# Performance work log

Hardware: AMD Instinct MI355X
Metric: run time of the kernel (lower is better)

## Reference

```python
import jax, jax.numpy as jnp
import numpy as np

N_NODES = 50000
N_EDGES = 500000
N_REL = 8
D = 128        # input_dim
A_DIM = 64     # attention_dim
D_OUT = 128    # output_dim


def setup_inputs() -> dict:
    key = jax.random.key(0)
    ks = jax.random.split(key, 10)
    h = jax.random.normal(ks[0], (N_NODES, D), jnp.float32)
    # relation gate tables: [R, 2*D, D]; first D rows act on dst (subject), last D on src (object)
    relations = jax.random.normal(ks[1], (N_REL, 2 * D, D), jnp.float32) * 0.05
    rel_attention = jax.random.normal(ks[2], (N_REL, A_DIM), jnp.float32) * 0.05
    W_a = jax.random.normal(ks[3], (A_DIM, 2 * D), jnp.float32) * 0.05
    b_a = jnp.zeros((A_DIM,), jnp.float32)
    W_lin = jax.random.normal(ks[4], (D_OUT, 2 * D), jnp.float32) * 0.05
    b_lin = jnp.zeros((D_OUT,), jnp.float32)
    src = jax.random.randint(ks[5], (N_EDGES,), 0, N_NODES, dtype=jnp.int32)
    dst = jax.random.randint(ks[6], (N_EDGES,), 0, N_NODES, dtype=jnp.int32)
    etype = jax.random.randint(ks[7], (N_EDGES,), 0, N_REL, dtype=jnp.int32)
    return {"h": h, "relations": relations, "rel_attention": rel_attention,
            "W_a": W_a, "b_a": b_a, "W_lin": W_lin, "b_lin": b_lin,
            "src": src, "dst": dst, "etype": etype}


def reference(h, relations, rel_attention, W_a, b_a, W_lin, b_lin, src, dst, etype):
    d = h.shape[-1]
    # --- gates: relation-indexed gather_mm (concat gate type) ---
    # Project every node through every relation once (R is small), then gather per edge.
    proj_dst = jnp.einsum('nd,rde->rne', h, relations[:, :d, :])   # [R, N, D] subject/dst side
    proj_src = jnp.einsum('nd,rde->rne', h, relations[:, d:, :])   # [R, N, D] object/src side
    gate = jax.nn.sigmoid(proj_dst[etype, dst] + proj_src[etype, src])  # [E, D]

    src_h = h[src]   # [E, D]
    dst_h = h[dst]   # [E, D]

    # --- gatv2 attention (predicates are zeroed in the module -> rel_attention[0]) ---
    a = jax.nn.leaky_relu(jnp.concatenate([dst_h, src_h], axis=-1) @ W_a.T + b_a)  # [E, A]
    score = (rel_attention[0] * a).sum(-1)  # [E]

    # --- edge_softmax over destination-node segments ---
    smax = jax.ops.segment_max(score, dst, num_segments=N_NODES)
    ex = jnp.exp(score - smax[dst])
    denom = jax.ops.segment_sum(ex, dst, num_segments=N_NODES)
    attn = ex / denom[dst]  # [E]

    # --- message = u_mul_e(h, attn*gate), reduce = sum over dst ---
    msg = src_h * (attn[:, None] * gate)                 # [E, D]
    h_N = jax.ops.segment_sum(msg, dst, num_segments=N_NODES)  # [N, D]

    # --- graphsage aggregate: LeakyReLU(W [h ; h_N] + b) ---
    out = jax.nn.leaky_relu(jnp.concatenate([h, h_N], axis=-1) @ W_lin.T + b_lin)
    return out
```

## Files before the change

### kernel.cpp

```cpp
#include <hip/hip_runtime.h>
#include <cstdint>
#include <cstddef>

constexpr int NNODES = 50000;
constexpr int NEDGES = 500000;
constexpr int NRELS  = 8;
constexpr int DIM    = 128;
constexpr int ADIM   = 64;
constexpr int TWOD   = 256;
constexpr int EPB    = 64;
constexpr float SLOPE = 0.01f;

constexpr int XPITCH = TWOD + 8;
constexpr int SPAD = NEDGES + 1024;

typedef __attribute__((ext_vector_type(8))) short short8;
typedef __attribute__((ext_vector_type(4))) float floatx4;

__device__ __forceinline__ unsigned short f2bf(float f) {
    unsigned u = __float_as_uint(f);
    unsigned r = u + 0x7FFFu + ((u >> 16) & 1u);
    return (unsigned short)(r >> 16);
}
__device__ __forceinline__ float bf2f(unsigned short b) {
    return __uint_as_float(((unsigned)b) << 16);
}
__device__ __forceinline__ float sigmoid_fast(float x) {
    return __builtin_amdgcn_rcpf(1.0f + __expf(-x));
}

typedef const __attribute__((address_space(1))) void* gas_ptr;
typedef __attribute__((address_space(3))) void* las_ptr;
__device__ __forceinline__ void gload_lds16(const void* g, void* l) {
    __builtin_amdgcn_global_load_lds((gas_ptr)g, (las_ptr)l, 16, 0, 0);
}

__global__ void k_init(int* __restrict__ histD, int* __restrict__ cursorD,
                       int* __restrict__ cnts) {
    int i = blockIdx.x * blockDim.x + threadIdx.x;
    int stride = gridDim.x * blockDim.x;
    for (int idx = i; idx < NNODES; idx += stride) { histD[idx] = 0; cursorD[idx] = 0; }
    if (i < 16) cnts[i] = 0;
}

__global__ __launch_bounds__(256) void k_prep(const float* __restrict__ rel,
                                              const float* __restrict__ W_lin,
                                              const float* __restrict__ W_a,
                                              unsigned short* __restrict__ relT,
                                              unsigned short* __restrict__ Wl,
                                              unsigned short* __restrict__ Wa16) {
    __shared__ float ls[64][65];
    int b = blockIdx.x, t = threadIdx.x;
    if (b < 64) {
        int r = b >> 3, tile = b & 7;
        int d0 = (tile >> 1) * 64, o0 = (tile & 1) * 64;
        const float* rp = rel + ((size_t)r * TWOD + d0) * DIM + o0;
#pragma unroll
        for (int u = 0; u < 16; u++) {
            int v = u * 256 + t;
            int j = v & 63, i = v >> 6;
            ls[i][j] = rp[(size_t)i * DIM + j];
        }
        __syncthreads();
        unsigned short* wp = relT + ((size_t)r * DIM + o0) * TWOD + d0;
#pragma unroll
        for (int u = 0; u < 16; u++) {
            int v = u * 256 + t;
            int ii = v & 63, jj = v >> 6;
            wp[(size_t)jj * TWOD + ii] = f2bf(ls[ii][jj]);
        }
    } else {
        int idx = (b - 64) * 256 + t;
        if (idx < DIM * TWOD) {
            Wl[idx] = f2bf(W_lin[idx]);
        } else {
            int j = idx - DIM * TWOD;
            if (j < ADIM * TWOD) Wa16[j] = f2bf(W_a[j]);
        }
    }
}

__global__ void k_h16(const float* __restrict__ h, unsigned short* __restrict__ h16) {
    int i = blockIdx.x * 256 + threadIdx.x;
    if (i < NNODES * DIM / 8) {
        const float4* hp = (const float4*)(h + (size_t)i * 8);
        float4 a = hp[0], b = hp[1];
        union { unsigned short us[8]; short8 s8; } pk;
        pk.us[0] = f2bf(a.x); pk.us[1] = f2bf(a.y); pk.us[2] = f2bf(a.z); pk.us[3] = f2bf(a.w);
        pk.us[4] = f2bf(b.x); pk.us[5] = f2bf(b.y); pk.us[6] = f2bf(b.z); pk.us[7] = f2bf(b.w);
        *(short8*)&h16[(size_t)i * 8] = pk.s8;
    }
}

__global__ void k_hist2(const int* __restrict__ ety, const int* __restrict__ dst,
                        int* __restrict__ cnt, int* __restrict__ histD) {
    __shared__ int hist[NRELS];
    int t = threadIdx.x;
    if (t < NRELS) hist[t] = 0;
    __syncthreads();
    int e = blockIdx.x * 256 + t;
    if (e < NEDGES) {
        atomicAdd(&hist[ety[e]], 1);
        atomicAdd(&histD[dst[e]], 1);
    }
    __syncthreads();
    if (t < NRELS && hist[t] > 0) atomicAdd(&cnt[t], hist[t]);
}

__global__ __launch_bounds__(1024) void k_scan(const int* __restrict__ histD,
                                               int* __restrict__ row_ptr,
                                               const int* __restrict__ cnt,
                                               int* __restrict__ offs,
                                               uint2* __restrict__ sMeta) {
    __shared__ int ls[1024];
    __shared__ int s_offs[NRELS + 1];
    __shared__ int s_cnt[NRELS];
    const int t = threadIdx.x;
    const int CH = (NNODES + 1023) / 1024;
    const int base = t * CH;
    int s = 0;
    for (int j = 0; j < CH; j++) { int i = base + j; if (i < NNODES) s += histD[i]; }
    ls[t] = s;
    __syncthreads();
    for (int off = 1; off < 1024; off <<= 1) {
        int v = (t >= off) ? ls[t - off] : 0;
        __syncthreads();
        ls[t] += v;
        __syncthreads();
    }
    int run = (t == 0) ? 0 : ls[t - 1];
    for (int j = 0; j < CH; j++) {
        int i = base + j;
        if (i < NNODES) { row_ptr[i] = run; run += histD[i]; }
    }
    if (t == 1023) row_ptr[NNODES] = ls[1023];
    if (t == 0) {
        int off = 0;
        for (int r = 0; r < NRELS; r++) {
            offs[r] = off; s_offs[r] = off; s_cnt[r] = cnt[r];
            off += ((cnt[r] + EPB - 1) / EPB) * EPB;
        }
        s_offs[NRELS] = off;
    }
    __syncthreads();
#pragma unroll
    for (int r = 0; r < NRELS; r++) {
        int s0 = s_offs[r] + s_cnt[r];
        int e0 = s_offs[r + 1 > NRELS ? NRELS : r + 1];
        for (int idx = s0 + t; idx < e0; idx += 1024) sMeta[idx] = make_uint2(0xFFFFFFFFu, 0u);
    }
    for (int idx = s_offs[NRELS] + t; idx < SPAD; idx += 1024)
        sMeta[idx] = make_uint2(0xFFFFFFFFu, 0u);
}

__global__ void k_escatter(const int* __restrict__ ety, const int* __restrict__ src,
                           const int* __restrict__ dst, const int* __restrict__ row_ptr,
                           const int* __restrict__ offs,
                           int* __restrict__ cursorD, int* __restrict__ cursorE,
                           uint2* __restrict__ sMeta) {
    __shared__ int hist[NRELS];
    __shared__ int basew[NRELS];
    int t = threadIdx.x;
    if (t < NRELS) hist[t] = 0;
    __syncthreads();
    int e = blockIdx.x * 256 + t;
    int r = -1, rank = 0, sn = 0, dn = 0;
    if (e < NEDGES) {
        r = ety[e]; sn = src[e]; dn = dst[e];
        rank = atomicAdd(&hist[r], 1);
    }
    __syncthreads();
    if (t < NRELS && hist[t] > 0) basew[t] = atomicAdd(&cursorE[t], hist[t]);
    __syncthreads();
    if (e < NEDGES) {
        int s = offs[r] + basew[r] + rank;
        int pos = row_ptr[dn] + atomicAdd(&cursorD[dn], 1);
        sMeta[s] = make_uint2((unsigned)sn | ((unsigned)dn << 16), (unsigned)pos);
    }
}

__global__ __launch_bounds__(256, 4) void k_gate_msg(
    const unsigned short* __restrict__ h16, const unsigned short* __restrict__ relT,
    const unsigned short* __restrict__ Wa16,
    const uint2* __restrict__ sMeta, const float* __restrict__ b_a,
    const float* __restrict__ ratt, const int* __restrict__ offs,
    unsigned short* __restrict__ msgbuf, float* __restrict__ scoreP) {
    __shared__ unsigned short Xs[EPB * 256];
    __shared__ int srcn_s[EPB];
    __shared__ int dstn_s[EPB];
    __shared__ int pos_s[EPB];
    __shared__ int val_s[EPB];
    __shared__ float scoreW[EPB][4];

    const int t = threadIdx.x;
    const int base = blockIdx.x * EPB;
    const int lane = t & 63;
    const int wave = t >> 6;

    if (t < EPB) {
        uint2 m2 = sMeta[base + t];
        int valid = (m2.x != 0xFFFFFFFFu);
        val_s[t] = valid;
        srcn_s[t] = valid ? (int)(m2.x & 0xFFFFu) : 0;
        dstn_s[t] = valid ? (int)(m2.x >> 16) : 0;
        pos_s[t] = valid ? (int)m2.y : 0;
    }
    __syncthreads();
    if (!val_s[0]) return;

    int r = 0;
#pragma unroll
    for (int i = 1; i < NRELS; i++) if (base >= offs[i]) r = i;

#pragma unroll
    for (int u = 0; u < 8; u++) {
        int j = wave * 8 + u;
        int row = j * 2 + (lane >> 5);
        int lu = (lane & 31) ^ (row & 7);
        int node = (lu < 16) ? dstn_s[row] : srcn_s[row];
        gload_lds16(&h16[(size_t)node * DIM + (lu & 15) * 8], &Xs[j * 512]);
    }

    const int q = lane >> 4;
    const int l16 = lane & 15;
    const int o16 = wave * 16 + l16;

    const unsigned short* bp0 = relT + ((size_t)r * DIM + (wave * 2 + 0) * 16 + l16) * TWOD + q * 8;
    const unsigned short* bp1 = relT + ((size_t)r * DIM + (wave * 2 + 1) * 16 + l16) * TWOD + q * 8;
    const unsigned short* wb  = Wa16 + (size_t)o16 * TWOD + q * 8;

    short8 B0p[8];
#pragma unroll
    for (int ks = 0; ks < 8; ks++) B0p[ks] = *(const short8*)(bp0 + ks * 32);
#pragma unroll
    for (int ks = 0; ks < 8; ks++) asm volatile("" :: "v"(B0p[ks]));

    __syncthreads();

    floatx4 acc[4][2];
    floatx4 accS[4];
#pragma unroll
    for (int m = 0; m < 4; m++) {
        acc[m][0] = (floatx4)(0.0f);
        acc[m][1] = (floatx4)(0.0f);
        accS[m] = (floatx4)(0.0f);
    }

#pragma unroll
    for (int ks = 0; ks < 8; ks++) {
        short8 B0 = B0p[ks];
        short8 B1 = *(const short8*)(bp1 + ks * 32);
        short8 BS = *(const short8*)(wb + ks * 32);
        short8 Af[4];
#pragma unroll
        for (int m = 0; m < 4; m++) {
            int row = m * 16 + l16;
            Af[m] = *(const short8*)&Xs[row * 256 + ((((ks * 4) + q) ^ (l16 & 7)) << 3)];
        }
#pragma unroll
        for (int m = 0; m < 4; m++) {
            acc[m][0] = __builtin_amdgcn_mfma_f32_16x16x32_bf16(Af[m], B0, acc[m][0], 0, 0, 0);
            acc[m][1] = __builtin_amdgcn_mfma_f32_16x16x32_bf16(Af[m], B1, acc[m][1], 0, 0, 0);
            accS[m]   = __builtin_amdgcn_mfma_f32_16x16x32_bf16(Af[m], BS, accS[m], 0, 0, 0);
        }
    }

    __syncthreads();

    {
        float ba = b_a[o16];
        float ra = ratt[o16];
#pragma unroll
        for (int m = 0; m < 4; m++) {
#pragma unroll
            for (int rg = 0; rg < 4; rg++) {
                float v = accS[m][rg] + ba;
                v = v > 0.0f ? v : SLOPE * v;
                v *= ra;
#pragma unroll
                for (int off = 8; off > 0; off >>= 1) v += __shfl_xor(v, off, 16);
                if (l16 == 0) scoreW[m * 16 + q * 4 + rg][wave] = v;
            }
        }
    }

#pragma unroll
    for (int m = 0; m < 4; m++) {
        int ib = m * 16 + q * 4;
#pragma unroll
        for (int nn = 0; nn < 2; nn++) {
            int o = (wave * 2 + nn) * 16 + l16;
            int uS = 16 + (o >> 3), uD = o >> 3, ofs = o & 7;
#pragma unroll
            for (int rg = 0; rg < 4; rg++) {
                int i = ib + rg;
                float g = sigmoid_fast(acc[m][nn][rg]);
                float sh = bf2f(Xs[i * 256 + ((uS ^ (i & 7)) << 3) + ofs]);
                Xs[i * 256 + ((uD ^ (i & 7)) << 3) + ofs] = f2bf(sh * g);
            }
        }
    }
    __syncthreads();

#pragma unroll
    for (int u = 0; u < 4; u++) {
        int v = u * 256 + t;
        int i = v >> 4;
        int c = v & 15;
        if (!val_s[i]) continue;
        short8 val = *(const short8*)&Xs[i * 256 + ((c ^ (i & 7)) << 3)];
        *(short8*)&msgbuf[(size_t)pos_s[i] * DIM + c * 8] = val;
    }
    if (t < EPB && val_s[t]) {
        scoreP[pos_s[t]] = scoreW[t][0] + scoreW[t][1] + scoreW[t][2] + scoreW[t][3];
    }
}

__global__ __launch_bounds__(256) void k_aggr(const unsigned short* __restrict__ msgbuf,
                                              const float* __restrict__ scoreP,
                                              const int* __restrict__ row_ptr,
                                              unsigned short* __restrict__ hN16) {
    int n = blockIdx.x * 4 + (threadIdx.x >> 6);
    int lane = threadIdx.x & 63;
    if (n >= NNODES) return;
    int p0 = row_ptr[n], p1 = row_ptr[n + 1];
    float a0 = 0.0f, a1 = 0.0f;
    if (p0 < p1) {
        float mx = -3.0e38f;
        for (int p = p0 + lane; p < p1; p += 64) mx = fmaxf(mx, scoreP[p]);
#pragma unroll
        for (int off = 32; off > 0; off >>= 1) mx = fmaxf(mx, __shfl_xor(mx, off));
        float sum = 0.0f;
        for (int p = p0 + lane; p < p1; p += 64) sum += __expf(scoreP[p] - mx);
#pragma unroll
        for (int off = 32; off > 0; off >>= 1) sum += __shfl_xor(sum, off);
        int p = p0;
        const unsigned short* mb = msgbuf + (size_t)lane * 2;
        for (; p + 4 <= p1; p += 4) {
            float w0 = __expf(scoreP[p + 0] - mx);
            float w1 = __expf(scoreP[p + 1] - mx);
            float w2 = __expf(scoreP[p + 2] - mx);
            float w3 = __expf(scoreP[p + 3] - mx);
            unsigned v0 = *(const unsigned*)&mb[(size_t)(p + 0) * DIM];
            unsigned v1 = *(const unsigned*)&mb[(size_t)(p + 1) * DIM];
            unsigned v2 = *(const unsigned*)&mb[(size_t)(p + 2) * DIM];
            unsigned v3 = *(const unsigned*)&mb[(size_t)(p + 3) * DIM];
            a0 = fmaf(w0, bf2f((unsigned short)(v0 & 0xFFFFu)), a0);
            a1 = fmaf(w0, bf2f((unsigned short)(v0 >> 16)), a1);
            a0 = fmaf(w1, bf2f((unsigned short)(v1 & 0xFFFFu)), a0);
            a1 = fmaf(w1, bf2f((unsigned short)(v1 >> 16)), a1);
            a0 = fmaf(w2, bf2f((unsigned short)(v2 & 0xFFFFu)), a0);
            a1 = fmaf(w2, bf2f((unsigned short)(v2 >> 16)), a1);
            a0 = fmaf(w3, bf2f((unsigned short)(v3 & 0xFFFFu)), a0);
            a1 = fmaf(w3, bf2f((unsigned short)(v3 >> 16)), a1);
        }
        for (; p < p1; p++) {
            float w = __expf(scoreP[p] - mx);
            unsigned v = *(const unsigned*)&mb[(size_t)p * DIM];
            a0 = fmaf(w, bf2f((unsigned short)(v & 0xFFFFu)), a0);
            a1 = fmaf(w, bf2f((unsigned short)(v >> 16)), a1);
        }
        float inv = __builtin_amdgcn_rcpf(sum);
        a0 *= inv; a1 *= inv;
    }
    unsigned o = (unsigned)f2bf(a0) | ((unsigned)f2bf(a1) << 16);
    *(unsigned*)&hN16[(size_t)n * DIM + lane * 2] = o;
}

__global__ __launch_bounds__(256) void k_out(const unsigned short* __restrict__ h16,
                                             const unsigned short* __restrict__ hN16,
                                             const unsigned short* __restrict__ Wl,
                                             const float* __restrict__ b_lin,
                                             float* __restrict__ out) {
    __shared__ unsigned short Xs[EPB * XPITCH];
    const int t = threadIdx.x;
    const int nb = blockIdx.x * 64;

#pragma unroll
    for (int u = 0; u < 8; u++) {
        int v = u * 256 + t;
        int i = v >> 5;
        int c = v & 31;
        int n = nb + i;
        if (n >= NNODES) n = NNODES - 1;
        const unsigned short* srcp = (c < 16) ? h16 : hN16;
        *(short8*)&Xs[i * XPITCH + c * 8] = *(const short8*)&srcp[(size_t)n * DIM + (c & 15) * 8];
    }

    const int wave = t >> 6;
    const int lane = t & 63;
    const int q = lane >> 4;
    const int l16 = lane & 15;

    short8 Bf[2][8];
#pragma unroll
    for (int nn = 0; nn < 2; nn++) {
        int o = (wave * 2 + nn) * 16 + l16;
        const unsigned short* bp = Wl + (size_t)o * TWOD + q * 8;
#pragma unroll
        for (int ks = 0; ks < 8; ks++) Bf[nn][ks] = *(const short8*)(bp + ks * 32);
    }

    __syncthreads();

    floatx4 acc[4][2];
#pragma unroll
    for (int m = 0; m < 4; m++)
#pragma unroll
        for (int nn = 0; nn < 2; nn++) acc[m][nn] = (floatx4)(0.0f);

#pragma unroll
    for (int ks = 0; ks < 8; ks++) {
        short8 Af[4];
        const unsigned short* xb = &Xs[l16 * XPITCH + ks * 32 + q * 8];
#pragma unroll
        for (int m = 0; m < 4; m++) Af[m] = *(const short8*)(xb + m * 16 * XPITCH);
#pragma unroll
        for (int m = 0; m < 4; m++)
#pragma unroll
            for (int nn = 0; nn < 2; nn++)
                acc[m][nn] = __builtin_amdgcn_mfma_f32_16x16x32_bf16(Af[m], Bf[nn][ks], acc[m][nn], 0, 0, 0);
    }

#pragma unroll
    for (int m = 0; m < 4; m++) {
        int ib = m * 16 + q * 4;
#pragma unroll
        for (int nn = 0; nn < 2; nn++) {
            int o = (wave * 2 + nn) * 16 + l16;
            float bl = b_lin[o];
#pragma unroll
            for (int rg = 0; rg < 4; rg++) {
                int n = nb + ib + rg;
                if (n < NNODES) {
                    float val = acc[m][nn][rg] + bl;
                    val = val > 0.0f ? val : SLOPE * val;
                    out[(size_t)n * DIM + o] = val;
                }
            }
        }
    }
}

extern "C" void kernel_launch(void* const* d_in, const int* in_sizes, int n_in,
                              void* d_out, int out_size, void* d_ws, size_t ws_size,
                              hipStream_t stream) {
    const float* h     = (const float*)d_in[0];
    const float* rel   = (const float*)d_in[1];
    const float* ratt  = (const float*)d_in[2];
    const float* W_a   = (const float*)d_in[3];
    const float* b_a   = (const float*)d_in[4];
    const float* W_lin = (const float*)d_in[5];
    const float* b_lin = (const float*)d_in[6];
    const int* src = (const int*)d_in[7];
    const int* dst = (const int*)d_in[8];
    const int* ety = (const int*)d_in[9];
    float* out = (float*)d_out;

    float* scoreP = (float*)d_ws;
    unsigned short* h16  = (unsigned short*)(scoreP + NEDGES);
    unsigned short* hN16 = h16 + (size_t)NNODES * DIM;
    unsigned short* relT = hN16 + (size_t)NNODES * DIM;
    unsigned short* Wl   = relT + (size_t)NRELS * DIM * TWOD;
    unsigned short* Wa16 = Wl + (size_t)DIM * TWOD;
    uint2* sMeta = (uint2*)(Wa16 + (size_t)ADIM * TWOD);
    int* row_ptr = (int*)(sMeta + SPAD);
    int* histD   = row_ptr + (NNODES + 1);
    int* cursorD = histD + NNODES;
    int* cnts    = cursorD + NNODES;
    int* offs    = cnts + 16;
    unsigned short* msgbuf = (unsigned short*)(((uintptr_t)(offs + 8) + 255) & ~(uintptr_t)255);

    k_init<<<256, 256, 0, stream>>>(histD, cursorD, cnts);
    k_prep<<<64 + (DIM * TWOD + ADIM * TWOD + 255) / 256, 256, 0, stream>>>(
        rel, W_lin, W_a, relT, Wl, Wa16);
    k_h16<<<(NNODES * DIM / 8 + 255) / 256, 256, 0, stream>>>(h, h16);
    k_hist2<<<(NEDGES + 255) / 256, 256, 0, stream>>>(ety, dst, cnts, histD);
    k_scan<<<1, 1024, 0, stream>>>(histD, row_ptr, cnts, offs, sMeta);
    k_escatter<<<(NEDGES + 255) / 256, 256, 0, stream>>>(
        ety, src, dst, row_ptr, offs, cursorD, cnts + 8, sMeta);
    k_gate_msg<<<(NEDGES + 8 * EPB + EPB - 1) / EPB, 256, 0, stream>>>(
        h16, relT, Wa16, sMeta, b_a, ratt, offs, msgbuf, scoreP);
    k_aggr<<<(NNODES + 3) / 4, 256, 0, stream>>>(msgbuf, scoreP, row_ptr, hN16);
    k_out<<<(NNODES + 63) / 64, 256, 0, stream>>>(h16, hN16, Wl, b_lin, out);
}
```

Before: 454.5 us.

## Fuse prep kernels and switch gate_msg to padded LDS with register prefetch

Merges the h-to-bf16 conversion and the edge histogram kernels into k_prep as extra block ranges, and moves the cursorD zeroing into k_scan, which removes two kernel launches and shrinks k_init. In k_gate_msg, the direct global-to-LDS loads with an XOR swizzle are replaced by ordinary vector loads into an LDS tile padded to a pitch of 264. The B operands for the first four k-steps of all three weight matrices are now prefetched into registers before the barrier. The fused launch puts extra LDS use and barriers into every k_prep block, and the padded layout may bring different bank conflicts and more register pressure.

```diff
diff --git a/kernel.cpp b/kernel.cpp
--- a/kernel.cpp
+++ b/kernel.cpp
@@ -29,27 +29,27 @@
     return __builtin_amdgcn_rcpf(1.0f + __expf(-x));
 }
 
-typedef const __attribute__((address_space(1))) void* gas_ptr;
-typedef __attribute__((address_space(3))) void* las_ptr;
-__device__ __forceinline__ void gload_lds16(const void* g, void* l) {
-    __builtin_amdgcn_global_load_lds((gas_ptr)g, (las_ptr)l, 16, 0, 0);
-}
-
-__global__ void k_init(int* __restrict__ histD, int* __restrict__ cursorD,
-                       int* __restrict__ cnts) {
+__global__ void k_init(int* __restrict__ histD, int* __restrict__ cnts) {
     int i = blockIdx.x * blockDim.x + threadIdx.x;
     int stride = gridDim.x * blockDim.x;
-    for (int idx = i; idx < NNODES; idx += stride) { histD[idx] = 0; cursorD[idx] = 0; }
+    for (int idx = i; idx < NNODES; idx += stride) histD[idx] = 0;
     if (i < 16) cnts[i] = 0;
 }
 
 __global__ __launch_bounds__(256) void k_prep(const float* __restrict__ rel,
                                               const float* __restrict__ W_lin,
                                               const float* __restrict__ W_a,
+                                              const float* __restrict__ h,
+                                              const int* __restrict__ ety,
+                                              const int* __restrict__ dst,
                                               unsigned short* __restrict__ relT,
                                               unsigned short* __restrict__ Wl,
-                                              unsigned short* __restrict__ Wa16) {
+                                              unsigned short* __restrict__ Wa16,
+                                              unsigned short* __restrict__ h16,
+                                              int* __restrict__ cnt,
+                                              int* __restrict__ histD) {
     __shared__ float ls[64][65];
+    __shared__ int hist[NRELS];
     int b = blockIdx.x, t = threadIdx.x;
     if (b < 64) {
         int r = b >> 3, tile = b & 7;
@@ -69,7 +69,7 @@
             int ii = v & 63, jj = v >> 6;
             wp[(size_t)jj * TWOD + ii] = f2bf(ls[ii][jj]);
         }
-    } else {
+    } else if (b < 256) {
         int idx = (b - 64) * 256 + t;
         if (idx < DIM * TWOD) {
             Wl[idx] = f2bf(W_lin[idx]);
@@ -77,38 +77,32 @@
             int j = idx - DIM * TWOD;
             if (j < ADIM * TWOD) Wa16[j] = f2bf(W_a[j]);
         }
-    }
-}
-
-__global__ void k_h16(const float* __restrict__ h, unsigned short* __restrict__ h16) {
-    int i = blockIdx.x * 256 + threadIdx.x;
-    if (i < NNODES * DIM / 8) {
-        const float4* hp = (const float4*)(h + (size_t)i * 8);
-        float4 a = hp[0], b = hp[1];
-        union { unsigned short us[8]; short8 s8; } pk;
-        pk.us[0] = f2bf(a.x); pk.us[1] = f2bf(a.y); pk.us[2] = f2bf(a.z); pk.us[3] = f2bf(a.w);
-        pk.us[4] = f2bf(b.x); pk.us[5] = f2bf(b.y); pk.us[6] = f2bf(b.z); pk.us[7] = f2bf(b.w);
-        *(short8*)&h16[(size_t)i * 8] = pk.s8;
-    }
-}
-
-__global__ void k_hist2(const int* __restrict__ ety, const int* __restrict__ dst,
-                        int* __restrict__ cnt, int* __restrict__ histD) {
-    __shared__ int hist[NRELS];
-    int t = threadIdx.x;
-    if (t < NRELS) hist[t] = 0;
-    __syncthreads();
-    int e = blockIdx.x * 256 + t;
-    if (e < NEDGES) {
-        atomicAdd(&hist[ety[e]], 1);
-        atomicAdd(&histD[dst[e]], 1);
-    }
-    __syncthreads();
-    if (t < NRELS && hist[t] > 0) atomicAdd(&cnt[t], hist[t]);
+    } else if (b < 3381) {
+        int i = (b - 256) * 256 + t;
+        if (i < NNODES * DIM / 8) {
+            const float4* hp = (const float4*)(h + (size_t)i * 8);
+            float4 a = hp[0], bb = hp[1];
+            union { unsigned short us[8]; short8 s8; } pk;
+            pk.us[0] = f2bf(a.x); pk.us[1] = f2bf(a.y); pk.us[2] = f2bf(a.z); pk.us[3] = f2bf(a.w);
+            pk.us[4] = f2bf(bb.x); pk.us[5] = f2bf(bb.y); pk.us[6] = f2bf(bb.z); pk.us[7] = f2bf(bb.w);
+            *(short8*)&h16[(size_t)i * 8] = pk.s8;
+        }
+    } else {
+        if (t < NRELS) hist[t] = 0;
+        __syncthreads();
+        int e = (b - 3381) * 256 + t;
+        if (e < NEDGES) {
+            atomicAdd(&hist[ety[e]], 1);
+            atomicAdd(&histD[dst[e]], 1);
+        }
+        __syncthreads();
+        if (t < NRELS && hist[t] > 0) atomicAdd(&cnt[t], hist[t]);
+    }
 }
 
 __global__ __launch_bounds__(1024) void k_scan(const int* __restrict__ histD,
                                                int* __restrict__ row_ptr,
+                                               int* __restrict__ cursorD,
                                                const int* __restrict__ cnt,
                                                int* __restrict__ offs,
                                                uint2* __restrict__ sMeta) {
@@ -131,7 +125,7 @@
     int run = (t == 0) ? 0 : ls[t - 1];
     for (int j = 0; j < CH; j++) {
         int i = base + j;
-        if (i < NNODES) { row_ptr[i] = run; run += histD[i]; }
+        if (i < NNODES) { row_ptr[i] = run; cursorD[i] = 0; run += histD[i]; }
     }
     if (t == 1023) row_ptr[NNODES] = ls[1023];
     if (t == 0) {
@@ -185,7 +179,7 @@
     const uint2* __restrict__ sMeta, const float* __restrict__ b_a,
     const float* __restrict__ ratt, const int* __restrict__ offs,
     unsigned short* __restrict__ msgbuf, float* __restrict__ scoreP) {
-    __shared__ unsigned short Xs[EPB * 256];
+    __shared__ unsigned short Xs[EPB * XPITCH];
     __shared__ int srcn_s[EPB];
     __shared__ int dstn_s[EPB];
     __shared__ int pos_s[EPB];
@@ -194,8 +188,6 @@
 
     const int t = threadIdx.x;
     const int base = blockIdx.x * EPB;
-    const int lane = t & 63;
-    const int wave = t >> 6;
 
     if (t < EPB) {
         uint2 m2 = sMeta[base + t];
@@ -214,13 +206,15 @@
 
 #pragma unroll
     for (int u = 0; u < 8; u++) {
-        int j = wave * 8 + u;
-        int row = j * 2 + (lane >> 5);
-        int lu = (lane & 31) ^ (row & 7);
-        int node = (lu < 16) ? dstn_s[row] : srcn_s[row];
-        gload_lds16(&h16[(size_t)node * DIM + (lu & 15) * 8], &Xs[j * 512]);
-    }
-
+        int v = u * 256 + t;
+        int i = v >> 5;
+        int c = v & 31;
+        int node = (c < 16) ? dstn_s[i] : srcn_s[i];
+        *(short8*)&Xs[i * XPITCH + c * 8] = *(const short8*)&h16[(size_t)node * DIM + (c & 15) * 8];
+    }
+
+    const int wave = t >> 6;
+    const int lane = t & 63;
     const int q = lane >> 4;
     const int l16 = lane & 15;
     const int o16 = wave * 16 + l16;
@@ -229,11 +223,13 @@
     const unsigned short* bp1 = relT + ((size_t)r * DIM + (wave * 2 + 1) * 16 + l16) * TWOD + q * 8;
     const unsigned short* wb  = Wa16 + (size_t)o16 * TWOD + q * 8;
 
-    short8 B0p[8];
-#pragma unroll
-    for (int ks = 0; ks < 8; ks++) B0p[ks] = *(const short8*)(bp0 + ks * 32);
-#pragma unroll
-    for (int ks = 0; ks < 8; ks++) asm volatile("" :: "v"(B0p[ks]));
+    short8 B0p[4], B1p[4], BSp[4];
+#pragma unroll
+    for (int ks = 0; ks < 4; ks++) {
+        B0p[ks] = *(const short8*)(bp0 + ks * 32);
+        B1p[ks] = *(const short8*)(bp1 + ks * 32);
+        BSp[ks] = *(const short8*)(wb + ks * 32);
+    }
 
     __syncthreads();
 
@@ -248,15 +244,13 @@
 
 #pragma unroll
     for (int ks = 0; ks < 8; ks++) {
-        short8 B0 = B0p[ks];
-        short8 B1 = *(const short8*)(bp1 + ks * 32);
-        short8 BS = *(const short8*)(wb + ks * 32);
+        short8 B0 = (ks < 4) ? B0p[ks & 3] : *(const short8*)(bp0 + ks * 32);
+        short8 B1 = (ks < 4) ? B1p[ks & 3] : *(const short8*)(bp1 + ks * 32);
+        short8 BS = (ks < 4) ? BSp[ks & 3] : *(const short8*)(wb + ks * 32);
         short8 Af[4];
-#pragma unroll
-        for (int m = 0; m < 4; m++) {
-            int row = m * 16 + l16;
-            Af[m] = *(const short8*)&Xs[row * 256 + ((((ks * 4) + q) ^ (l16 & 7)) << 3)];
-        }
+        const unsigned short* xb = &Xs[l16 * XPITCH + ks * 32 + q * 8];
+#pragma unroll
+        for (int m = 0; m < 4; m++) Af[m] = *(const short8*)(xb + m * 16 * XPITCH);
 #pragma unroll
         for (int m = 0; m < 4; m++) {
             acc[m][0] = __builtin_amdgcn_mfma_f32_16x16x32_bf16(Af[m], B0, acc[m][0], 0, 0, 0);
@@ -290,13 +284,12 @@
 #pragma unroll
         for (int nn = 0; nn < 2; nn++) {
             int o = (wave * 2 + nn) * 16 + l16;
-            int uS = 16 + (o >> 3), uD = o >> 3, ofs = o & 7;
 #pragma unroll
             for (int rg = 0; rg < 4; rg++) {
                 int i = ib + rg;
                 float g = sigmoid_fast(acc[m][nn][rg]);
-                float sh = bf2f(Xs[i * 256 + ((uS ^ (i & 7)) << 3) + ofs]);
-                Xs[i * 256 + ((uD ^ (i & 7)) << 3) + ofs] = f2bf(sh * g);
+                float sh = bf2f(Xs[i * XPITCH + DIM + o]);
+                Xs[i * XPITCH + o] = f2bf(sh * g);
             }
         }
     }
@@ -308,7 +301,7 @@
         int i = v >> 4;
         int c = v & 15;
         if (!val_s[i]) continue;
-        short8 val = *(const short8*)&Xs[i * 256 + ((c ^ (i & 7)) << 3)];
+        short8 val = *(const short8*)&Xs[i * XPITCH + c * 8];
         *(short8*)&msgbuf[(size_t)pos_s[i] * DIM + c * 8] = val;
     }
     if (t < EPB && val_s[t]) {
@@ -471,12 +464,10 @@
     int* offs    = cnts + 16;
     unsigned short* msgbuf = (unsigned short*)(((uintptr_t)(offs + 8) + 255) & ~(uintptr_t)255);
 
-    k_init<<<256, 256, 0, stream>>>(histD, cursorD, cnts);
-    k_prep<<<64 + (DIM * TWOD + ADIM * TWOD + 255) / 256, 256, 0, stream>>>(
-        rel, W_lin, W_a, relT, Wl, Wa16);
-    k_h16<<<(NNODES * DIM / 8 + 255) / 256, 256, 0, stream>>>(h, h16);
-    k_hist2<<<(NEDGES + 255) / 256, 256, 0, stream>>>(ety, dst, cnts, histD);
-    k_scan<<<1, 1024, 0, stream>>>(histD, row_ptr, cnts, offs, sMeta);
+    k_init<<<196, 256, 0, stream>>>(histD, cnts);
+    k_prep<<<5335, 256, 0, stream>>>(rel, W_lin, W_a, h, ety, dst,
+                                     relT, Wl, Wa16, h16, cnts, histD);
+    k_scan<<<1, 1024, 0, stream>>>(histD, row_ptr, cursorD, cnts, offs, sMeta);
     k_escatter<<<(NEDGES + 255) / 256, 256, 0, stream>>>(
         ety, src, dst, row_ptr, offs, cursorD, cnts + 8, sMeta);
     k_gate_msg<<<(NEDGES + 8 * EPB + EPB - 1) / EPB, 256, 0, stream>>>(
```

New measurement: 468.2 us. +3.0%, slower.
